# Kernel optimization log

Hardware: AMD Instinct MI355X
Metric: run time of the kernel (lower is better)

The kernel has to match this reference:

```python
import jax, jax.numpy as jnp
from jax import lax
import numpy as np

B, CIN, COUT, N, H, W = 16, 64, 64, 8, 128, 128


def setup_inputs() -> dict:
    key = jax.random.key(0)
    ks = jax.random.split(key, 6)
    s = 0.05
    return {
        "x": jax.random.normal(ks[0], (B, CIN, H, W), dtype=jnp.float32),
        "condition": jax.random.normal(ks[1], (B, CIN), dtype=jnp.float32),
        "filt_w": jax.random.normal(ks[2], (N, COUT, CIN, 3, 3), dtype=jnp.float32) * s,
        "filt_b": jax.random.normal(ks[3], (N, COUT), dtype=jnp.float32) * s,
        "sel_w": jax.random.normal(ks[4], (N, CIN), dtype=jnp.float32) * s,
        "sel_b": jax.random.normal(ks[5], (N,), dtype=jnp.float32) * s,
    }


def reference(x, condition, filt_w, filt_b, sel_w, sel_b):
    b = x.shape[0]
    # condition selector: Linear(in_channels -> num_conditions) + softmax
    logits = condition.reshape(b, -1) @ sel_w.T + sel_b          # [B, N]
    weights = jax.nn.softmax(logits, axis=-1)                    # [B, N]

    n, cout, cin, kh, kw = filt_w.shape
    # Run all N branch convs in ONE conv by stacking filters on the output-channel axis.
    kern = filt_w.reshape(n * cout, cin, kh, kw)
    y = lax.conv_general_dilated(
        x, kern, window_strides=(1, 1), padding="SAME",
        dimension_numbers=("NCHW", "OIHW", "NCHW"))              # [B, N*COUT, H, W]
    h, w = y.shape[-2], y.shape[-1]
    y = y.reshape(b, n, cout, h, w) + filt_b.reshape(1, n, cout, 1, 1)
    # softmax-gated sum over the N branches
    out = jnp.einsum("bn,bnohw->bohw", weights, y)
    return out
```

## Files before the change

kernel.cpp:

```cpp
#include <hip/hip_runtime.h>
#include <stdint.h>

#define BATCH 16
#define CIN   64
#define COUT  64
#define NBR   8
#define HH    128
#define WW    128
#define XBH   130
#define XBW   130
#define PSTR  68
#define NTILES 1024

typedef __attribute__((ext_vector_type(8)))  short short8;
typedef __attribute__((ext_vector_type(16))) float f32x16;

__device__ __forceinline__ unsigned int f2bf_hi(float f) {
    union { float f; uint32_t u; } v; v.f = f;
    return (v.u + 0x8000u) >> 16;
}
__device__ __forceinline__ unsigned short f2bf(float f) {
    union { float f; uint32_t u; } v; v.f = f;
    uint32_t u = v.u;
    return (unsigned short)((u + 0x7FFFu + ((u >> 16) & 1u)) >> 16);
}
__device__ __forceinline__ short8 gld_frag(const unsigned short* p) {
    union { uint4 u; short8 s; } t;
    t.u = *(const uint4*)p;
    return t.s;
}
__device__ __forceinline__ short8 lds_frag(const unsigned short* p) {
    union { uint2 u[2]; short8 s; } t;
    t.u[0] = *(const uint2*)p;
    t.u[1] = *(const uint2*)(p + 4);
    return t.s;
}
__device__ __forceinline__ void gload_lds16(const unsigned short* g, unsigned short* l) {
    __builtin_amdgcn_global_load_lds(
        (const __attribute__((address_space(1))) unsigned int*)g,
        (__attribute__((address_space(3))) unsigned int*)l, 16, 0, 0);
}

__global__ __launch_bounds__(256)
void k_pc(const float* __restrict__ cond,
          const float* __restrict__ sel_w,
          const float* __restrict__ sel_b,
          const float* __restrict__ filt_w,
          const float* __restrict__ filt_b,
          const float* __restrict__ x,
          unsigned short* __restrict__ wfilt,
          float* __restrict__ cbias,
          unsigned short* __restrict__ xb) {
    __shared__ float4 lw4[NBR * 144];
    __shared__ float lg[NBR];
    const int tid = threadIdx.x;

    if (blockIdx.x < NTILES) {
        float* lw = (float*)lw4;
        const int blk = blockIdx.x;
        const int b = blk >> 6, o = blk & 63;

        const float4* src4 = (const float4*)filt_w;
        #pragma unroll
        for (int i = tid; i < NBR * 144; i += 256)
            lw4[i] = src4[((i / 144) * COUT + o) * 144 + (i % 144)];

        {
            const int lane = tid & 63, w = tid >> 6;
            const float c0 = cond[b * CIN + lane];
            #pragma unroll
            for (int k = 0; k < 2; ++k) {
                const int n = w + k * 4;
                float p = c0 * sel_w[n * CIN + lane];
                #pragma unroll
                for (int off = 32; off > 0; off >>= 1)
                    p += __shfl_down(p, off, 64);
                if (lane == 0) lg[n] = p + sel_b[n];
            }
        }
        __syncthreads();

        float w8[NBR];
        {
            float m = -1e30f;
            #pragma unroll
            for (int n = 0; n < NBR; ++n) m = fmaxf(m, lg[n]);
            float s = 0.f;
            #pragma unroll
            for (int n = 0; n < NBR; ++n) { w8[n] = __expf(lg[n] - m); s += w8[n]; }
            const float inv = 1.f / s;
            #pragma unroll
            for (int n = 0; n < NBR; ++n) w8[n] *= inv;
        }

        #pragma unroll
        for (int idx = tid; idx < 576; idx += 256) {
            const int t = idx >> 6, c = idx & 63;
            float acc = 0.f;
            #pragma unroll
            for (int n = 0; n < NBR; ++n)
                acc += w8[n] * lw[n * 576 + c * 9 + t];
            wfilt[(((long)(b * 9 + t) * COUT + o) << 6) + c] = f2bf(acc);
        }
        if (tid == 0) {
            float ab = 0.f;
            #pragma unroll
            for (int n = 0; n < NBR; ++n) ab += w8[n] * filt_b[n * COUT + o];
            cbias[b * COUT + o] = ab;
        }
    } else {
        const int id = blockIdx.x - NTILES;
        const int hp = id % XBH;
        const int b  = id / XBH;
        unsigned short* dst = xb + (long)(b * XBH + hp) * XBW * PSTR;
        const bool zrow = (hp == 0) || (hp == XBH - 1);
        const int h = hp - 1;
        const long cs = (long)HH * WW;

        for (int t = tid; t < XBW * 8; t += 256) {
            const int wp = t >> 3, q = t & 7;
            uint4 v; v.x = v.y = v.z = v.w = 0u;
            if (!zrow && wp != 0 && wp != XBW - 1) {
                const float* px = x + (((long)(b * CIN + q * 8)) * HH + h) * WW + (wp - 1);
                v.x = f2bf_hi(px[0])      | (f2bf_hi(px[cs])     << 16);
                v.y = f2bf_hi(px[2 * cs]) | (f2bf_hi(px[3 * cs]) << 16);
                v.z = f2bf_hi(px[4 * cs]) | (f2bf_hi(px[5 * cs]) << 16);
                v.w = f2bf_hi(px[6 * cs]) | (f2bf_hi(px[7 * cs]) << 16);
            }
            unsigned short* dp = dst + wp * PSTR + q * 8;
            uint2 u0, u1;
            u0.x = v.x; u0.y = v.y; u1.x = v.z; u1.y = v.w;
            *(uint2*)dp       = u0;
            *(uint2*)(dp + 4) = u1;
            if (q == 7) {
                uint2 z; z.x = z.y = 0u;
                *(uint2*)(dst + wp * PSTR + 64) = z;
            }
        }
    }
}

#define RT 8
#define WT 32
#define SLABW 34
#define SLABR 10
#define ROWUS (SLABW * PSTR)
#define NCHUNK (SLABR * ROWUS / 8)

__global__ __launch_bounds__(256, 3)
void k_conv(const unsigned short* __restrict__ xb,
            const unsigned short* __restrict__ wfilt,
            const float* __restrict__ cbias,
            float* __restrict__ out) {
    __shared__ unsigned short lx[SLABR * ROWUS];

    const int b  = blockIdx.z;
    const int h0 = blockIdx.y * RT;
    const int w0 = blockIdx.x * WT;
    const int tid = threadIdx.x;

    const unsigned short* srcb = xb + ((long)(b * XBH + h0) * XBW + w0) * PSTR;
    #pragma unroll
    for (int k = 0; k < 12; ++k) {
        const int t = tid + k * 256;
        if (t < NCHUNK) {
            const int row = t / 289;
            const int rc  = t - row * 289;
            gload_lds16(srcb + (long)row * (XBW * PSTR) + rc * 8, lx + t * 8);
        }
    }

    const int lane = tid & 63;
    const int wave = tid >> 6;
    const int l31  = lane & 31;
    const int lh   = lane >> 5;
    const int r0   = wave * 2;

    const unsigned short* wf = wfilt + (long)b * 9 * COUT * CIN;

    short8 A0[4], A1[4];
    #pragma unroll
    for (int cc = 0; cc < 4; ++cc) {
        A0[cc] = gld_frag(wf + l31 * CIN + cc * 16 + lh * 8);
        A1[cc] = gld_frag(wf + (32 + l31) * CIN + cc * 16 + lh * 8);
    }

    f32x16 acc00, acc01, acc10, acc11;
    #pragma unroll
    for (int i = 0; i < 16; ++i) {
        const int m = (i & 3) + 8 * (i >> 2) + 4 * lh;
        const float b0 = cbias[b * COUT + m];
        const float b1 = cbias[b * COUT + 32 + m];
        acc00[i] = b0; acc01[i] = b0;
        acc10[i] = b1; acc11[i] = b1;
    }

    __syncthreads();

    #pragma unroll
    for (int tap = 0; tap < 9; ++tap) {
        short8 nA0[4], nA1[4];
        if (tap < 8) {
            const unsigned short* wn = wf + (long)(tap + 1) * COUT * CIN;
            #pragma unroll
            for (int cc = 0; cc < 4; ++cc) {
                nA0[cc] = gld_frag(wn + l31 * CIN + cc * 16 + lh * 8);
                nA1[cc] = gld_frag(wn + (32 + l31) * CIN + cc * 16 + lh * 8);
            }
        }
        const int kh = tap / 3, kw = tap % 3;
        #pragma unroll
        for (int cc = 0; cc < 4; ++cc) {
            const int kofs = cc * 16 + lh * 8;
            short8 b0 = lds_frag(&lx[((r0     + kh) * SLABW + l31 + kw) * PSTR + kofs]);
            short8 b1 = lds_frag(&lx[((r0 + 1 + kh) * SLABW + l31 + kw) * PSTR + kofs]);
            acc00 = __builtin_amdgcn_mfma_f32_32x32x16_bf16(A0[cc], b0, acc00, 0, 0, 0);
            acc01 = __builtin_amdgcn_mfma_f32_32x32x16_bf16(A0[cc], b1, acc01, 0, 0, 0);
            acc10 = __builtin_amdgcn_mfma_f32_32x32x16_bf16(A1[cc], b0, acc10, 0, 0, 0);
            acc11 = __builtin_amdgcn_mfma_f32_32x32x16_bf16(A1[cc], b1, acc11, 0, 0, 0);
        }
        #pragma unroll
        for (int cc = 0; cc < 4; ++cc) { A0[cc] = nA0[cc]; A1[cc] = nA1[cc]; }
    }

    #pragma unroll
    for (int cb = 0; cb < 2; ++cb) {
        #pragma unroll
        for (int pb = 0; pb < 2; ++pb) {
            const f32x16 v = cb == 0 ? (pb == 0 ? acc00 : acc01)
                                     : (pb == 0 ? acc10 : acc11);
            const int hrow = h0 + r0 + pb;
            float* op = out + (((long)(b * COUT + cb * 32) * HH + hrow) * WW + w0 + l31);
            #pragma unroll
            for (int i = 0; i < 16; ++i) {
                const int m = (i & 3) + 8 * (i >> 2) + 4 * lh;
                op[(long)m * HH * WW] = v[i];
            }
        }
    }
}

extern "C" void kernel_launch(void* const* d_in, const int* in_sizes, int n_in,
                              void* d_out, int out_size, void* d_ws, size_t ws_size,
                              hipStream_t stream) {
    const float* x      = (const float*)d_in[0];
    const float* cond   = (const float*)d_in[1];
    const float* filt_w = (const float*)d_in[2];
    const float* filt_b = (const float*)d_in[3];
    const float* sel_w  = (const float*)d_in[4];
    const float* sel_b  = (const float*)d_in[5];
    float* out = (float*)d_out;

    float*          cbias = (float*)d_ws;
    unsigned short* wfilt = (unsigned short*)((char*)d_ws + 4096);
    unsigned short* xb    = (unsigned short*)((char*)d_ws + 4096 + 1179648);

    k_pc<<<NTILES + BATCH * XBH, 256, 0, stream>>>(cond, sel_w, sel_b, filt_w, filt_b, x,
                                                   wfilt, cbias, xb);

    dim3 grid(WW / WT, HH / RT, BATCH);
    k_conv<<<grid, 256, 0, stream>>>(xb, wfilt, cbias, out);
}
```

Measured before the change: 181.2 us.

## Split output channels across waves and halve row tile per block

Each block now covers 4 output rows instead of 8. The four waves are split 2x2 over row pairs and 32-channel output halves, so each wave keeps 2 accumulators instead of 4. This cuts register pressure and LDS footprint, which allows 4 blocks per CU and doubles the grid. In exchange the halo overhead per block rises (6 slab rows loaded for 4 output rows), and each weight fragment is reused across fewer MFMAs.

Measured after the change: 183.7 us. No clear change (+1.4%).

```diff
diff --git a/kernel.cpp b/kernel.cpp
--- a/kernel.cpp
+++ b/kernel.cpp
@@ -140,14 +140,14 @@
     }
 }
 
-#define RT 8
+#define RT 4
 #define WT 32
 #define SLABW 34
-#define SLABR 10
+#define SLABR 6
 #define ROWUS (SLABW * PSTR)
 #define NCHUNK (SLABR * ROWUS / 8)
 
-__global__ __launch_bounds__(256, 3)
+__global__ __launch_bounds__(256, 4)
 void k_conv(const unsigned short* __restrict__ xb,
             const unsigned short* __restrict__ wfilt,
             const float* __restrict__ cbias,
@@ -161,7 +161,7 @@
 
     const unsigned short* srcb = xb + ((long)(b * XBH + h0) * XBW + w0) * PSTR;
     #pragma unroll
-    for (int k = 0; k < 12; ++k) {
+    for (int k = 0; k < 7; ++k) {
         const int t = tid + k * 256;
         if (t < NCHUNK) {
             const int row = t / 289;
@@ -174,39 +174,35 @@
     const int wave = tid >> 6;
     const int l31  = lane & 31;
     const int lh   = lane >> 5;
-    const int r0   = wave * 2;
-
-    const unsigned short* wf = wfilt + (long)b * 9 * COUT * CIN;
-
-    short8 A0[4], A1[4];
-    #pragma unroll
-    for (int cc = 0; cc < 4; ++cc) {
-        A0[cc] = gld_frag(wf + l31 * CIN + cc * 16 + lh * 8);
-        A1[cc] = gld_frag(wf + (32 + l31) * CIN + cc * 16 + lh * 8);
-    }
-
-    f32x16 acc00, acc01, acc10, acc11;
+    const int wp   = wave & 1;
+    const int wc   = wave >> 1;
+    const int r0   = wp * 2;
+
+    const unsigned short* wf = wfilt + (long)b * 9 * COUT * CIN + wc * 32 * CIN;
+
+    short8 A[4];
+    #pragma unroll
+    for (int cc = 0; cc < 4; ++cc)
+        A[cc] = gld_frag(wf + l31 * CIN + cc * 16 + lh * 8);
+
+    f32x16 acc0, acc1;
     #pragma unroll
     for (int i = 0; i < 16; ++i) {
         const int m = (i & 3) + 8 * (i >> 2) + 4 * lh;
-        const float b0 = cbias[b * COUT + m];
-        const float b1 = cbias[b * COUT + 32 + m];
-        acc00[i] = b0; acc01[i] = b0;
-        acc10[i] = b1; acc11[i] = b1;
+        const float bb = cbias[b * COUT + wc * 32 + m];
+        acc0[i] = bb; acc1[i] = bb;
     }
 
     __syncthreads();
 
     #pragma unroll
     for (int tap = 0; tap < 9; ++tap) {
-        short8 nA0[4], nA1[4];
+        short8 nA[4];
         if (tap < 8) {
             const unsigned short* wn = wf + (long)(tap + 1) * COUT * CIN;
             #pragma unroll
-            for (int cc = 0; cc < 4; ++cc) {
-                nA0[cc] = gld_frag(wn + l31 * CIN + cc * 16 + lh * 8);
-                nA1[cc] = gld_frag(wn + (32 + l31) * CIN + cc * 16 + lh * 8);
-            }
+            for (int cc = 0; cc < 4; ++cc)
+                nA[cc] = gld_frag(wn + l31 * CIN + cc * 16 + lh * 8);
         }
         const int kh = tap / 3, kw = tap % 3;
         #pragma unroll
@@ -214,28 +210,22 @@
             const int kofs = cc * 16 + lh * 8;
             short8 b0 = lds_frag(&lx[((r0     + kh) * SLABW + l31 + kw) * PSTR + kofs]);
             short8 b1 = lds_frag(&lx[((r0 + 1 + kh) * SLABW + l31 + kw) * PSTR + kofs]);
-            acc00 = __builtin_amdgcn_mfma_f32_32x32x16_bf16(A0[cc], b0, acc00, 0, 0, 0);
-            acc01 = __builtin_amdgcn_mfma_f32_32x32x16_bf16(A0[cc], b1, acc01, 0, 0, 0);
-            acc10 = __builtin_amdgcn_mfma_f32_32x32x16_bf16(A1[cc], b0, acc10, 0, 0, 0);
-            acc11 = __builtin_amdgcn_mfma_f32_32x32x16_bf16(A1[cc], b1, acc11, 0, 0, 0);
-        }
-        #pragma unroll
-        for (int cc = 0; cc < 4; ++cc) { A0[cc] = nA0[cc]; A1[cc] = nA1[cc]; }
-    }
-
-    #pragma unroll
-    for (int cb = 0; cb < 2; ++cb) {
-        #pragma unroll
-        for (int pb = 0; pb < 2; ++pb) {
-            const f32x16 v = cb == 0 ? (pb == 0 ? acc00 : acc01)
-                                     : (pb == 0 ? acc10 : acc11);
-            const int hrow = h0 + r0 + pb;
-            float* op = out + (((long)(b * COUT + cb * 32) * HH + hrow) * WW + w0 + l31);
-            #pragma unroll
-            for (int i = 0; i < 16; ++i) {
-                const int m = (i & 3) + 8 * (i >> 2) + 4 * lh;
-                op[(long)m * HH * WW] = v[i];
-            }
+            acc0 = __builtin_amdgcn_mfma_f32_32x32x16_bf16(A[cc], b0, acc0, 0, 0, 0);
+            acc1 = __builtin_amdgcn_mfma_f32_32x32x16_bf16(A[cc], b1, acc1, 0, 0, 0);
+        }
+        #pragma unroll
+        for (int cc = 0; cc < 4; ++cc) A[cc] = nA[cc];
+    }
+
+    #pragma unroll
+    for (int pb = 0; pb < 2; ++pb) {
+        const f32x16 v = pb == 0 ? acc0 : acc1;
+        const int hrow = h0 + r0 + pb;
+        float* op = out + (((long)(b * COUT + wc * 32) * HH + hrow) * WW + w0 + l31);
+        #pragma unroll
+        for (int i = 0; i < 16; ++i) {
+            const int m = (i & 3) + 8 * (i >> 2) + 4 * lh;
+            op[(long)m * HH * WW] = v[i];
         }
     }
 }
```
